# Optimization experiments

Hardware: AMD Instinct MI355X
Metric: run time of the kernel (lower is better)

Reference implementation:

```python
import jax, jax.numpy as jnp
import numpy as np

B, N, C, D = 64, 1024, 128, 64

def setup_inputs() -> dict:
    key = jax.random.key(0)
    ks = jax.random.split(key, 7)
    # kaiming_normal_ on weights (fan_in = C), default zero-ish biases kept as Linear default uniform; use small uniform
    std = float(np.sqrt(2.0 / C))
    bb = float(1.0 / np.sqrt(C))
    return {
        "x": jax.random.normal(ks[0], (B, N, C), jnp.float32),
        "Wq": jax.random.normal(ks[1], (C, D), jnp.float32) * std,
        "bq": jax.random.uniform(ks[2], (D,), jnp.float32, -bb, bb),
        "Wk": jax.random.normal(ks[3], (C, D), jnp.float32) * std,
        "bk": jax.random.uniform(ks[4], (D,), jnp.float32, -bb, bb),
        "Wv": jax.random.normal(ks[5], (C, D), jnp.float32) * std,
        "bv": jax.random.uniform(ks[6], (D,), jnp.float32, -bb, bb),
    }

def reference(x, Wq, bq, Wk, bk, Wv, bv):
    q = jax.nn.relu(jnp.einsum('bnc,cd->bnd', x, Wq) + bq)  # [B,N,D]
    k = jax.nn.relu(jnp.einsum('bnc,cd->bnd', x, Wk) + bk)
    v = jax.nn.relu(jnp.einsum('bnc,cd->bnd', x, Wv) + bv)
    scores = jnp.einsum('bnd,bmd->bnm', q, k) / jnp.sqrt(jnp.asarray(D, q.dtype))
    attn = jax.nn.softmax(scores, axis=-1)
    out = jnp.einsum('bnm,bmd->bnd', attn, v)
    return out + q
```

## Files before the change

kernel.cpp:

```cpp
#include <hip/hip_runtime.h>
#include <hip/hip_bf16.h>


#define Bsz 64
#define Nsz 1024
#define Csz 128
#define Dsz 64

typedef __attribute__((ext_vector_type(8))) short short8;
typedef __attribute__((ext_vector_type(4))) float f32x4;

__device__ __forceinline__ unsigned short f2bf(float f) {
    union { float f; unsigned u; } v; v.f = f;
    unsigned r = v.u + 0x7FFF + ((v.u >> 16) & 1);
    return (unsigned short)(r >> 16);
}
__device__ __forceinline__ float bf2f(unsigned short h) {
    union { unsigned u; float f; } v; v.u = ((unsigned)h) << 16;
    return v.f;
}
__device__ __forceinline__ unsigned pack_bf16rn(float lo, float hi) {
    unsigned ulo = __float_as_uint(lo) + 0x8000u;
    unsigned uhi = __float_as_uint(hi) + 0x8000u;
    return __builtin_amdgcn_perm(uhi, ulo, 0x07060302u);
}

#define SCq (0.125f * 1.44269504f)
#define INV_SC (1.0f / (0.125f * 1.44269504f))

__global__ __launch_bounds__(256) void wprep_kernel(
    const float* __restrict__ Wq, const float* __restrict__ Wk,
    const float* __restrict__ Wv, unsigned short* __restrict__ wfrag)
{
    int t = blockIdx.x * 256 + threadIdx.x;
    int lane = t & 63, ksi = (t >> 6) & 3, dt = t >> 8;
    int l16 = lane & 15, quad = lane >> 4;
    int d = dt * 16 + l16;
    int c0 = ksi * 32 + quad * 8;
    short8 h8, l8, k8, v8;
    #pragma unroll
    for (int j = 0; j < 8; j++) {
        float w = Wq[(c0 + j) * Dsz + d];
        unsigned short h = f2bf(w);
        h8[j] = (short)h;
        l8[j] = (short)f2bf(w - bf2f(h));
        k8[j] = (short)f2bf(Wk[(c0 + j) * Dsz + d]);
        v8[j] = (short)f2bf(Wv[(c0 + j) * Dsz + d]);
    }
    int idx = (dt * 4 + ksi) * 64 + lane;
    ((short8*)wfrag)[0 * 1024 + idx] = h8;
    ((short8*)wfrag)[1 * 1024 + idx] = l8;
    ((short8*)wfrag)[2 * 1024 + idx] = k8;
    ((short8*)wfrag)[3 * 1024 + idx] = v8;
}

__global__ __launch_bounds__(256) void qkv_kernel(
    const float* __restrict__ x, const unsigned short* __restrict__ wfrag,
    const float* __restrict__ bq, const float* __restrict__ bk,
    const float* __restrict__ bv,
    unsigned short* __restrict__ qs, unsigned short* __restrict__ ks2,
    unsigned short* __restrict__ vt2)
{
    __shared__ short xh[8192];
    __shared__ short xl[8192];
    const int t    = threadIdx.x;
    const int lane = t & 63;
    const int l16  = lane & 15, quad = lane >> 4;
    const int dt   = t >> 6;
    const long rowbase = (long)blockIdx.x * 64;
    const int d = dt * 16 + l16;

    short8 wqh[4], wql[4], wkf[4], wvf[4];
    #pragma unroll
    for (int ksi = 0; ksi < 4; ksi++) {
        int idx = (dt * 4 + ksi) * 64 + lane;
        wqh[ksi] = ((const short8*)wfrag)[0 * 1024 + idx];
        wql[ksi] = ((const short8*)wfrag)[1 * 1024 + idx];
        wkf[ksi] = ((const short8*)wfrag)[2 * 1024 + idx];
        wvf[ksi] = ((const short8*)wfrag)[3 * 1024 + idx];
    }

    {
        const int row = t & 63;
        const float* xrow = x + (rowbase + row) * Csz;
        #pragma unroll
        for (int p = 0; p < 4; p++) {
            int cb = (t >> 6) + p * 4;
            float4 a = *(const float4*)(xrow + cb * 8);
            float4 bb = *(const float4*)(xrow + cb * 8 + 4);
            float f[8] = {a.x, a.y, a.z, a.w, bb.x, bb.y, bb.z, bb.w};
            short8 hi, lo;
            #pragma unroll
            for (int i = 0; i < 8; i++) {
                unsigned short h = f2bf(f[i]);
                hi[i] = (short)h;
                lo[i] = (short)f2bf(f[i] - bf2f(h));
            }
            int unit = ((row >> 4) * 4 + (cb >> 2)) * 64 + ((row & 15) | ((cb & 3) << 4));
            *(short8*)&xh[unit * 8] = hi;
            *(short8*)&xl[unit * 8] = lo;
        }
    }
    __syncthreads();

    f32x4 aq[4], ak[4], av[4];
    #pragma unroll
    for (int i = 0; i < 4; i++) {
        aq[i] = (f32x4){0.f, 0.f, 0.f, 0.f};
        ak[i] = (f32x4){0.f, 0.f, 0.f, 0.f};
        av[i] = (f32x4){0.f, 0.f, 0.f, 0.f};
    }
    #pragma unroll
    for (int ksi = 0; ksi < 4; ksi++) {
        #pragma unroll
        for (int rt = 0; rt < 4; rt++) {
            short8 ah = *(const short8*)&xh[((rt * 4 + ksi) * 64 + lane) * 8];
            short8 al = *(const short8*)&xl[((rt * 4 + ksi) * 64 + lane) * 8];
            aq[rt] = __builtin_amdgcn_mfma_f32_16x16x32_bf16(ah, wqh[ksi], aq[rt], 0, 0, 0);
            aq[rt] = __builtin_amdgcn_mfma_f32_16x16x32_bf16(al, wqh[ksi], aq[rt], 0, 0, 0);
            aq[rt] = __builtin_amdgcn_mfma_f32_16x16x32_bf16(ah, wql[ksi], aq[rt], 0, 0, 0);
            ak[rt] = __builtin_amdgcn_mfma_f32_16x16x32_bf16(ah, wkf[ksi], ak[rt], 0, 0, 0);
            av[rt] = __builtin_amdgcn_mfma_f32_16x16x32_bf16(ah, wvf[ksi], av[rt], 0, 0, 0);
        }
    }

    const float bqd = bq[d], bkd = bk[d], bvd = bv[d];
    const long b  = rowbase >> 10;
    const int  kt = (int)((rowbase >> 6) & 15);

    const int half  = dt >> 1;
    const int quadk = ((dt & 1) << 1) | (l16 >> 3);
    const int jk    = l16 & 7;
    unsigned short* kbase = ks2 + ((((long)(b * 16 + kt) * 4) * 2 + half) * 64) * 8;

    float vv[4][4];
    #pragma unroll
    for (int rt = 0; rt < 4; rt++) {
        #pragma unroll
        for (int r = 0; r < 4; r++) {
            long n = rowbase + rt * 16 + quad * 4 + r;
            float q = fmaxf(aq[rt][r] + bqd, 0.f);
            float k = fmaxf(ak[rt][r] + bkd, 0.f);
            vv[r][rt] = fmaxf(av[rt][r] + bvd, 0.f);
            qs[n * Dsz + d] = f2bf(q * SCq);
            kbase[((long)rt * 2 * 64 + quadk * 16 + quad * 4 + r) * 8 + jk] = f2bf(k);
        }
    }
    const int ck = quad >> 1;
    const int quadp = (quad & 1) * 2;
    long vidx = (((long)(b * 16 + kt) * 4 + dt) * 2 + ck) * 64 + quadp * 16 + l16;
    uint4 o0 = make_uint4(pack_bf16rn(vv[0][0], vv[0][1]), pack_bf16rn(vv[0][2], vv[0][3]),
                          pack_bf16rn(vv[1][0], vv[1][1]), pack_bf16rn(vv[1][2], vv[1][3]));
    uint4 o1 = make_uint4(pack_bf16rn(vv[2][0], vv[2][1]), pack_bf16rn(vv[2][2], vv[2][3]),
                          pack_bf16rn(vv[3][0], vv[3][1]), pack_bf16rn(vv[3][2], vv[3][3]));
    ((uint4*)vt2)[vidx]      = o0;
    ((uint4*)vt2)[vidx + 16] = o1;
}

__global__ __launch_bounds__(256) void attn_kernel(
    const unsigned short* __restrict__ qs,
    const unsigned short* __restrict__ ks2,
    const unsigned short* __restrict__ vt2,
    float* __restrict__ out)
{
    __shared__ short Pl[4][32][72];

    const int t    = threadIdx.x;
    const int wave = t >> 6;
    const int lane = t & 63;
    const int l16  = lane & 15;
    const int quad = lane >> 4;
    const int b    = blockIdx.x & 63;
    const int qh   = blockIdx.x >> 6;
    const int qbase = qh * 128 + wave * 32;

    const short8* ks8 = (const short8*)ks2 + (long)b * (16 * 4 * 2 * 64);
    const short8* vt8 = (const short8*)vt2 + (long)b * (16 * 4 * 2 * 64);

    short8 aq[2][2];
    #pragma unroll
    for (int s = 0; s < 2; s++) {
        const unsigned short* qp = qs + ((long)b * Nsz + qbase + s * 16 + l16) * Dsz + quad * 8;
        aq[s][0] = *(const short8*)(qp);
        aq[s][1] = *(const short8*)(qp + 32);
    }

    f32x4 O[2][4];
    float lsum[2][4];
    #pragma unroll
    for (int s = 0; s < 2; s++)
        #pragma unroll
        for (int i = 0; i < 4; i++) { O[s][i] = (f32x4){0.f,0.f,0.f,0.f}; lsum[s][i] = 0.f; }

    short8 kf[4][2];
    #pragma unroll
    for (int kb = 0; kb < 4; kb++) {
        kf[kb][0] = ks8[(kb * 2 + 0) * 64 + lane];
        kf[kb][1] = ks8[(kb * 2 + 1) * 64 + lane];
    }

    for (int kt = 0; kt < 16; kt++) {
        short8 bvf[2][4];
        #pragma unroll
        for (int cb = 0; cb < 4; cb++) {
            bvf[0][cb] = vt8[((long)kt * 8 + cb * 2 + 0) * 64 + lane];
            bvf[1][cb] = vt8[((long)kt * 8 + cb * 2 + 1) * 64 + lane];
        }

        f32x4 sc[2][4];
        #pragma unroll
        for (int s = 0; s < 2; s++) {
            #pragma unroll
            for (int kb = 0; kb < 4; kb++) {
                f32x4 z = (f32x4){0.f, 0.f, 0.f, 0.f};
                z = __builtin_amdgcn_mfma_f32_16x16x32_bf16(aq[s][0], kf[kb][0], z, 0, 0, 0);
                z = __builtin_amdgcn_mfma_f32_16x16x32_bf16(aq[s][1], kf[kb][1], z, 0, 0, 0);
                sc[s][kb] = z;
            }
        }

        short8 kf2[4][2];
        {
            int ktn = (kt + 1) & 15;
            #pragma unroll
            for (int kb = 0; kb < 4; kb++) {
                kf2[kb][0] = ks8[((long)ktn * 8 + kb * 2 + 0) * 64 + lane];
                kf2[kb][1] = ks8[((long)ktn * 8 + kb * 2 + 1) * 64 + lane];
            }
        }

        #pragma unroll
        for (int s = 0; s < 2; s++) {
            #pragma unroll
            for (int r = 0; r < 4; r++) {
                float p0 = __builtin_amdgcn_exp2f(sc[s][0][r]);
                float p1 = __builtin_amdgcn_exp2f(sc[s][1][r]);
                float p2 = __builtin_amdgcn_exp2f(sc[s][2][r]);
                float p3 = __builtin_amdgcn_exp2f(sc[s][3][r]);
                lsum[s][r] += (p0 + p1) + (p2 + p3);
                *(uint2*)&Pl[wave][s * 16 + quad * 4 + r][l16 * 4] =
                    make_uint2(pack_bf16rn(p0, p1), pack_bf16rn(p2, p3));
            }
        }

        #pragma unroll
        for (int ck = 0; ck < 2; ck++) {
            #pragma unroll
            for (int s = 0; s < 2; s++) {
                short8 ap = *(const short8*)&Pl[wave][s * 16 + l16][ck * 32 + quad * 8];
                #pragma unroll
                for (int cb = 0; cb < 4; cb++) {
                    O[s][cb] = __builtin_amdgcn_mfma_f32_16x16x32_bf16(ap, bvf[ck][cb], O[s][cb], 0, 0, 0);
                }
            }
        }

        #pragma unroll
        for (int kb = 0; kb < 4; kb++) { kf[kb][0] = kf2[kb][0]; kf[kb][1] = kf2[kb][1]; }
    }

    #pragma unroll
    for (int s = 0; s < 2; s++)
        #pragma unroll
        for (int r = 0; r < 4; r++)
            #pragma unroll
            for (int off = 1; off < 16; off <<= 1)
                lsum[s][r] += __shfl_xor(lsum[s][r], off);

    #pragma unroll
    for (int s = 0; s < 2; s++) {
        #pragma unroll
        for (int r = 0; r < 4; r++) {
            float rl = 1.0f / lsum[s][r];
            long nrow = (long)b * Nsz + qbase + s * 16 + quad * 4 + r;
            #pragma unroll
            for (int cb = 0; cb < 4; cb++) {
                int d = cb * 16 + l16;
                float qv = bf2f(qs[nrow * Dsz + d]) * INV_SC;
                out[nrow * Dsz + d] = O[s][cb][r] * rl + qv;
            }
        }
    }
}

extern "C" void kernel_launch(void* const* d_in, const int* in_sizes, int n_in,
                              void* d_out, int out_size, void* d_ws, size_t ws_size,
                              hipStream_t stream) {
    const float* x  = (const float*)d_in[0];
    const float* Wq = (const float*)d_in[1];
    const float* bq = (const float*)d_in[2];
    const float* Wk = (const float*)d_in[3];
    const float* bk = (const float*)d_in[4];
    const float* Wv = (const float*)d_in[5];
    const float* bv = (const float*)d_in[6];
    float* out = (float*)d_out;

    char* ws = (char*)d_ws;
    unsigned short* qsc   = (unsigned short*)ws;
    unsigned short* ks2   = (unsigned short*)(ws + 0x1000000);
    unsigned short* vt2   = (unsigned short*)(ws + 0x2000000);
    unsigned short* wfrag = (unsigned short*)(ws + 0x3000000);

    wprep_kernel<<<dim3(4), dim3(256), 0, stream>>>(Wq, Wk, Wv, wfrag);
    qkv_kernel<<<dim3(1024), dim3(256), 0, stream>>>(
        x, wfrag, bq, bk, bv, qsc, ks2, vt2);
    attn_kernel<<<dim3(512), dim3(256), 0, stream>>>(
        qsc, ks2, vt2, out);
}
```

Measured before the change: 121.8 us.

## Stage QKV outputs through LDS for coalesced stores; widen attention waves to 64 rows

The QKV kernel now writes q, k and v tiles into shared memory first, then emits them as coalesced 16-byte global stores instead of scattered 2-byte writes. The attention kernel switches to 2 waves per block, each handling 64 query rows. This doubles K/V fragment reuse per global load, and K loads are double-buffered via a ping-pong register array. The epilogue stages the normalized output through LDS to write float4 rows and read q residuals vectorized. The cost is higher register pressure from the larger per-wave accumulators, and fewer waves per block.

```diff
diff --git a/kernel.cpp b/kernel.cpp
--- a/kernel.cpp
+++ b/kernel.cpp
@@ -61,8 +61,9 @@
     unsigned short* __restrict__ qs, unsigned short* __restrict__ ks2,
     unsigned short* __restrict__ vt2)
 {
-    __shared__ short xh[8192];
-    __shared__ short xl[8192];
+    __shared__ short lds[16384];
+    short* xh = lds;
+    short* xl = lds + 8192;
     const int t    = threadIdx.x;
     const int lane = t & 63;
     const int l16  = lane & 15, quad = lane >> 4;
@@ -128,42 +129,55 @@
     const long b  = rowbase >> 10;
     const int  kt = (int)((rowbase >> 6) & 15);
 
-    const int half  = dt >> 1;
-    const int quadk = ((dt & 1) << 1) | (l16 >> 3);
-    const int jk    = l16 & 7;
-    unsigned short* kbase = ks2 + ((((long)(b * 16 + kt) * 4) * 2 + half) * 64) * 8;
+    __syncthreads();
+    short* stq = lds;
+    short* stk = lds + 4608;
+    short* stv = lds + 9216;
 
     float vv[4][4];
     #pragma unroll
     for (int rt = 0; rt < 4; rt++) {
         #pragma unroll
         for (int r = 0; r < 4; r++) {
-            long n = rowbase + rt * 16 + quad * 4 + r;
+            int nl = rt * 16 + quad * 4 + r;
             float q = fmaxf(aq[rt][r] + bqd, 0.f);
             float k = fmaxf(ak[rt][r] + bkd, 0.f);
             vv[r][rt] = fmaxf(av[rt][r] + bvd, 0.f);
-            qs[n * Dsz + d] = f2bf(q * SCq);
-            kbase[((long)rt * 2 * 64 + quadk * 16 + quad * 4 + r) * 8 + jk] = f2bf(k);
-        }
-    }
-    const int ck = quad >> 1;
-    const int quadp = (quad & 1) * 2;
-    long vidx = (((long)(b * 16 + kt) * 4 + dt) * 2 + ck) * 64 + quadp * 16 + l16;
-    uint4 o0 = make_uint4(pack_bf16rn(vv[0][0], vv[0][1]), pack_bf16rn(vv[0][2], vv[0][3]),
-                          pack_bf16rn(vv[1][0], vv[1][1]), pack_bf16rn(vv[1][2], vv[1][3]));
-    uint4 o1 = make_uint4(pack_bf16rn(vv[2][0], vv[2][1]), pack_bf16rn(vv[2][2], vv[2][3]),
-                          pack_bf16rn(vv[3][0], vv[3][1]), pack_bf16rn(vv[3][2], vv[3][3]));
-    ((uint4*)vt2)[vidx]      = o0;
-    ((uint4*)vt2)[vidx + 16] = o1;
-}
-
-__global__ __launch_bounds__(256) void attn_kernel(
+            stq[nl * 72 + d] = (short)f2bf(q * SCq);
+            stk[nl * 72 + d] = (short)f2bf(k);
+        }
+    }
+    #pragma unroll
+    for (int r = 0; r < 4; r++) {
+        int slot = (dt * 2 + (quad >> 1)) * 64 + (((quad & 1) << 1) | (r >> 1)) * 16 + l16;
+        uint2 pk = make_uint2(pack_bf16rn(vv[r][0], vv[r][1]),
+                              pack_bf16rn(vv[r][2], vv[r][3]));
+        *(uint2*)&stv[slot * 8 + (r & 1) * 4] = pk;
+    }
+    __syncthreads();
+
+    const long tbase = (long)(b * 16 + kt) * 512;
+    #pragma unroll
+    for (int i = 0; i < 2; i++) {
+        int sidx = i * 256 + t;
+        int row = sidx >> 3, g = sidx & 7;
+        short8 vq = *(const short8*)&stq[row * 72 + g * 8];
+        ((short8*)qs)[(rowbase + row) * 8 + g] = vq;
+        int kb = sidx >> 7, rem = sidx & 127, half = rem >> 6, lam = rem & 63;
+        short8 vk = *(const short8*)&stk[(kb * 16 + (lam & 15)) * 72 + half * 32 + (lam >> 4) * 8];
+        ((short8*)ks2)[tbase + kb * 128 + half * 64 + lam] = vk;
+        short8 v8 = *(const short8*)&stv[sidx * 8];
+        ((short8*)vt2)[tbase + sidx] = v8;
+    }
+}
+
+__global__ __launch_bounds__(128) void attn_kernel(
     const unsigned short* __restrict__ qs,
     const unsigned short* __restrict__ ks2,
     const unsigned short* __restrict__ vt2,
     float* __restrict__ out)
 {
-    __shared__ short Pl[4][32][72];
+    __shared__ short Pl[2][64][72];
 
     const int t    = threadIdx.x;
     const int wave = t >> 6;
@@ -171,41 +185,40 @@
     const int l16  = lane & 15;
     const int quad = lane >> 4;
     const int b    = blockIdx.x & 63;
-    const int qh   = blockIdx.x >> 6;
-    const int qbase = qh * 128 + wave * 32;
-
-    const short8* ks8 = (const short8*)ks2 + (long)b * (16 * 4 * 2 * 64);
-    const short8* vt8 = (const short8*)vt2 + (long)b * (16 * 4 * 2 * 64);
-
-    short8 aq[2][2];
-    #pragma unroll
-    for (int s = 0; s < 2; s++) {
+    const int qo   = blockIdx.x >> 6;
+    const int qbase = qo * 128 + wave * 64;
+
+    const short8* ks8 = (const short8*)ks2 + (long)b * 8192;
+    const short8* vt8 = (const short8*)vt2 + (long)b * 8192;
+
+    short8 aq[4][2];
+    #pragma unroll
+    for (int s = 0; s < 4; s++) {
         const unsigned short* qp = qs + ((long)b * Nsz + qbase + s * 16 + l16) * Dsz + quad * 8;
         aq[s][0] = *(const short8*)(qp);
         aq[s][1] = *(const short8*)(qp + 32);
     }
 
-    f32x4 O[2][4];
-    float lsum[2][4];
-    #pragma unroll
-    for (int s = 0; s < 2; s++)
+    f32x4 O[4][4];
+    float lsum[4][4];
+    #pragma unroll
+    for (int s = 0; s < 4; s++)
         #pragma unroll
         for (int i = 0; i < 4; i++) { O[s][i] = (f32x4){0.f,0.f,0.f,0.f}; lsum[s][i] = 0.f; }
 
-    short8 kf[4][2];
+    short8 kf[2][4][2];
     #pragma unroll
     for (int kb = 0; kb < 4; kb++) {
-        kf[kb][0] = ks8[(kb * 2 + 0) * 64 + lane];
-        kf[kb][1] = ks8[(kb * 2 + 1) * 64 + lane];
+        kf[0][kb][0] = ks8[(kb * 2 + 0) * 64 + lane];
+        kf[0][kb][1] = ks8[(kb * 2 + 1) * 64 + lane];
     }
 
     for (int kt = 0; kt < 16; kt++) {
-        short8 bvf[2][4];
-        #pragma unroll
-        for (int cb = 0; cb < 4; cb++) {
-            bvf[0][cb] = vt8[((long)kt * 8 + cb * 2 + 0) * 64 + lane];
-            bvf[1][cb] = vt8[((long)kt * 8 + cb * 2 + 1) * 64 + lane];
-        }
+        const int cur = kt & 1;
+        short8 bvf0[4];
+        #pragma unroll
+        for (int cb = 0; cb < 4; cb++)
+            bvf0[cb] = vt8[((long)kt * 8 + cb * 2 + 0) * 64 + lane];
 
         f32x4 sc[2][4];
         #pragma unroll
@@ -213,22 +226,19 @@
             #pragma unroll
             for (int kb = 0; kb < 4; kb++) {
                 f32x4 z = (f32x4){0.f, 0.f, 0.f, 0.f};
-                z = __builtin_amdgcn_mfma_f32_16x16x32_bf16(aq[s][0], kf[kb][0], z, 0, 0, 0);
-                z = __builtin_amdgcn_mfma_f32_16x16x32_bf16(aq[s][1], kf[kb][1], z, 0, 0, 0);
+                z = __builtin_amdgcn_mfma_f32_16x16x32_bf16(aq[s][0], kf[cur][kb][0], z, 0, 0, 0);
+                z = __builtin_amdgcn_mfma_f32_16x16x32_bf16(aq[s][1], kf[cur][kb][1], z, 0, 0, 0);
                 sc[s][kb] = z;
             }
         }
-
-        short8 kf2[4][2];
         {
             int ktn = (kt + 1) & 15;
             #pragma unroll
             for (int kb = 0; kb < 4; kb++) {
-                kf2[kb][0] = ks8[((long)ktn * 8 + kb * 2 + 0) * 64 + lane];
-                kf2[kb][1] = ks8[((long)ktn * 8 + kb * 2 + 1) * 64 + lane];
-            }
-        }
-
+                kf[1 - cur][kb][0] = ks8[((long)ktn * 8 + kb * 2 + 0) * 64 + lane];
+                kf[1 - cur][kb][1] = ks8[((long)ktn * 8 + kb * 2 + 1) * 64 + lane];
+            }
+        }
         #pragma unroll
         for (int s = 0; s < 2; s++) {
             #pragma unroll
@@ -242,43 +252,77 @@
                     make_uint2(pack_bf16rn(p0, p1), pack_bf16rn(p2, p3));
             }
         }
-
-        #pragma unroll
-        for (int ck = 0; ck < 2; ck++) {
-            #pragma unroll
-            for (int s = 0; s < 2; s++) {
-                short8 ap = *(const short8*)&Pl[wave][s * 16 + l16][ck * 32 + quad * 8];
-                #pragma unroll
-                for (int cb = 0; cb < 4; cb++) {
-                    O[s][cb] = __builtin_amdgcn_mfma_f32_16x16x32_bf16(ap, bvf[ck][cb], O[s][cb], 0, 0, 0);
-                }
-            }
-        }
-
-        #pragma unroll
-        for (int kb = 0; kb < 4; kb++) { kf[kb][0] = kf2[kb][0]; kf[kb][1] = kf2[kb][1]; }
-    }
-
-    #pragma unroll
-    for (int s = 0; s < 2; s++)
+        #pragma unroll
+        for (int s = 0; s < 2; s++) {
+            #pragma unroll
+            for (int kb = 0; kb < 4; kb++) {
+                f32x4 z = (f32x4){0.f, 0.f, 0.f, 0.f};
+                z = __builtin_amdgcn_mfma_f32_16x16x32_bf16(aq[s + 2][0], kf[cur][kb][0], z, 0, 0, 0);
+                z = __builtin_amdgcn_mfma_f32_16x16x32_bf16(aq[s + 2][1], kf[cur][kb][1], z, 0, 0, 0);
+                sc[s][kb] = z;
+            }
+        }
+        #pragma unroll
+        for (int s = 0; s < 2; s++) {
+            #pragma unroll
+            for (int r = 0; r < 4; r++) {
+                float p0 = __builtin_amdgcn_exp2f(sc[s][0][r]);
+                float p1 = __builtin_amdgcn_exp2f(sc[s][1][r]);
+                float p2 = __builtin_amdgcn_exp2f(sc[s][2][r]);
+                float p3 = __builtin_amdgcn_exp2f(sc[s][3][r]);
+                lsum[s + 2][r] += (p0 + p1) + (p2 + p3);
+                *(uint2*)&Pl[wave][(s + 2) * 16 + quad * 4 + r][l16 * 4] =
+                    make_uint2(pack_bf16rn(p0, p1), pack_bf16rn(p2, p3));
+            }
+        }
+        short8 bvf1[4];
+        #pragma unroll
+        for (int cb = 0; cb < 4; cb++)
+            bvf1[cb] = vt8[((long)kt * 8 + cb * 2 + 1) * 64 + lane];
+
+        #pragma unroll
+        for (int s = 0; s < 4; s++) {
+            short8 ap0 = *(const short8*)&Pl[wave][s * 16 + l16][0 * 32 + quad * 8];
+            #pragma unroll
+            for (int cb = 0; cb < 4; cb++)
+                O[s][cb] = __builtin_amdgcn_mfma_f32_16x16x32_bf16(ap0, bvf0[cb], O[s][cb], 0, 0, 0);
+            short8 ap1 = *(const short8*)&Pl[wave][s * 16 + l16][1 * 32 + quad * 8];
+            #pragma unroll
+            for (int cb = 0; cb < 4; cb++)
+                O[s][cb] = __builtin_amdgcn_mfma_f32_16x16x32_bf16(ap1, bvf1[cb], O[s][cb], 0, 0, 0);
+        }
+    }
+
+    #pragma unroll
+    for (int s = 0; s < 4; s++)
         #pragma unroll
         for (int r = 0; r < 4; r++)
             #pragma unroll
             for (int off = 1; off < 16; off <<= 1)
                 lsum[s][r] += __shfl_xor(lsum[s][r], off);
 
-    #pragma unroll
-    for (int s = 0; s < 2; s++) {
+    float* fst = (float*)&Pl[wave][0][0];
+    #pragma unroll
+    for (int s = 0; s < 4; s++) {
         #pragma unroll
         for (int r = 0; r < 4; r++) {
             float rl = 1.0f / lsum[s][r];
-            long nrow = (long)b * Nsz + qbase + s * 16 + quad * 4 + r;
-            #pragma unroll
-            for (int cb = 0; cb < 4; cb++) {
-                int d = cb * 16 + l16;
-                float qv = bf2f(qs[nrow * Dsz + d]) * INV_SC;
-                out[nrow * Dsz + d] = O[s][cb][r] * rl + qv;
-            }
+            #pragma unroll
+            for (int cb = 0; cb < 4; cb++)
+                fst[(quad * 4 + r) * 68 + cb * 16 + l16] = O[s][cb][r] * rl;
+        }
+        #pragma unroll
+        for (int j = 0; j < 4; j++) {
+            int vidx = j * 64 + lane;
+            int row = vidx >> 4, dp = (vidx & 15) * 4;
+            f32x4 ov = *(const f32x4*)&fst[row * 68 + dp];
+            long nrow = (long)b * Nsz + qbase + s * 16 + row;
+            uint2 qv = *(const uint2*)(qs + nrow * Dsz + dp);
+            ov[0] += bf2f((unsigned short)(qv.x)) * INV_SC;
+            ov[1] += bf2f((unsigned short)(qv.x >> 16)) * INV_SC;
+            ov[2] += bf2f((unsigned short)(qv.y)) * INV_SC;
+            ov[3] += bf2f((unsigned short)(qv.y >> 16)) * INV_SC;
+            *(f32x4*)(out + nrow * Dsz + dp) = ov;
         }
     }
 }
@@ -304,6 +348,6 @@
     wprep_kernel<<<dim3(4), dim3(256), 0, stream>>>(Wq, Wk, Wv, wfrag);
     qkv_kernel<<<dim3(1024), dim3(256), 0, stream>>>(
         x, wfrag, bq, bk, bv, qsc, ks2, vt2);
-    attn_kernel<<<dim3(512), dim3(256), 0, stream>>>(
+    attn_kernel<<<dim3(512), dim3(128), 0, stream>>>(
         qsc, ks2, vt2, out);
 }
```

Result: slower. 167.5 us (+37.5%).
